# Optimization experiments

Hardware: AMD Instinct MI355X
Metric: run time of the kernel (lower is better)

## Reference

```python
import jax, jax.numpy as jnp
import numpy as np

EPS = 1e-12


def agnn_layer(x, row, col, num_nodes):
    """AGNN propagation with beta frozen at 1.0 (requires_grad=False in source).
    alpha_ij = softmax_{j in N(i)} ( beta * cos(x_i, x_j) ); out_i = sum_j alpha_ij * x_j.
    row = destination node of each edge (segment id), col = source node.
    """
    xn = x / (jnp.linalg.norm(x, axis=-1, keepdims=True) + EPS)  # unit-norm features
    score = jnp.sum(xn[row] * xn[col], axis=-1)                   # [E] beta=1 * cos sim
    smax = jax.ops.segment_max(score, row, num_segments=num_nodes)
    e = jnp.exp(score - smax[row])                                # stable softmax numerator
    denom = jax.ops.segment_sum(e, row, num_segments=num_nodes)
    alpha = e / jnp.maximum(denom[row], EPS)                      # [E]
    out = jax.ops.segment_sum(alpha[:, None] * x[col], row, num_segments=num_nodes)
    return out


def setup_inputs() -> dict:
    key = jax.random.key(0)
    ks = jax.random.split(key, 8)
    N, E = 100000, 1600000
    IN_DIM, HID, OUT_DIM = 128, 64, 64
    x = jax.random.normal(ks[0], (N, IN_DIM), dtype=jnp.float32)
    edge_row = jnp.sort(jax.random.randint(ks[1], (E,), 0, N))
    edge_col = jax.random.randint(ks[2], (E,), 0, N)
    # Linear params (PyTorch nn.Linear style: y = x @ W.T + b)
    s1 = 1.0 / np.sqrt(IN_DIM)
    W1 = jax.random.uniform(ks[3], (HID, IN_DIM), jnp.float32, -s1, s1)
    b1 = jax.random.uniform(ks[4], (HID,), jnp.float32, -s1, s1)
    s2 = 1.0 / np.sqrt(HID)
    W2 = jax.random.uniform(ks[5], (OUT_DIM, HID), jnp.float32, -s2, s2)
    b2 = jax.random.uniform(ks[6], (OUT_DIM,), jnp.float32, -s2, s2)
    return {"x": x, "edge_row": edge_row, "edge_col": edge_col,
            "W1": W1, "b1": b1, "W2": W2, "b2": b2}


def reference(x, edge_row, edge_col, W1, b1, W2, b2):
    N = x.shape[0]
    h = jax.nn.relu(x @ W1.T + b1)
    for _ in range(4):  # 4 frozen-beta AGNN layers
        h = jax.nn.relu(agnn_layer(h, edge_row, edge_col, N))
    return h @ W2.T + b2
```

## Files before the change

kernel.cpp:

```cpp
#include <hip/hip_runtime.h>


typedef float v2f __attribute__((ext_vector_type(2)));

#define DEV_INLINE __device__ __forceinline__

DEV_INLINE v2f bf2(unsigned u) {
    v2f r;
    r.x = __uint_as_float(u << 16);
    r.y = __uint_as_float(u & 0xffff0000u);
    return r;
}

DEV_INLINE unsigned pack_bf16_2(float a, float b) {
    unsigned ua = __float_as_uint(a); ua += 0x7fffu + ((ua >> 16) & 1u);
    unsigned ub = __float_as_uint(b); ub += 0x7fffu + ((ub >> 16) & 1u);
    return (ua >> 16) | (ub & 0xffff0000u);
}

template <int CTRL>
DEV_INLINE float dpp_add(float v) {
    int sh = __builtin_amdgcn_update_dpp(0, __float_as_int(v), CTRL, 0xF, 0xF, true);
    return v + __int_as_float(sh);
}
DEV_INLINE float group8_sum_bcast(float v) {
    float r = dpp_add<0x111>(v);
    r = dpp_add<0x112>(r);
    r = dpp_add<0x114>(r);
    return __int_as_float(__builtin_amdgcn_ds_swizzle(__float_as_int(r), 0x00F8));
}

__global__ __launch_bounds__(256) void build_rowptr(const int* __restrict__ row,
                                                    int* __restrict__ ptr,
                                                    int N, int E) {
    int i = blockIdx.x * blockDim.x + threadIdx.x;
    if (i > N) return;
    int lo = 0, hi = E;
    while (lo < hi) {
        int mid = (lo + hi) >> 1;
        if (row[mid] < i) lo = mid + 1; else hi = mid;
    }
    ptr[i] = lo;
}

__global__ __launch_bounds__(256) void gemm1_relu(const float* __restrict__ x,
                                                  const float* __restrict__ W1,
                                                  const float* __restrict__ b1,
                                                  unsigned short* __restrict__ xn,
                                                  float* __restrict__ nrm,
                                                  int N) {
    __shared__ __align__(16) float Wt[64 * 64];
    __shared__ __align__(16) float xT[64 * 64];
    const int tid  = threadIdx.x;
    const int tx   = tid & 15;
    const int ty   = tid >> 4;
    const int base = blockIdx.x * 64;

    float4 b4 = ((const float4*)b1)[tx];
    float4 acc[4];
    acc[0] = b4; acc[1] = b4; acc[2] = b4; acc[3] = b4;

    for (int kc = 0; kc < 128; kc += 64) {
        if (kc) __syncthreads();
        const float4* W4 = (const float4*)W1;
        for (int idx = tid; idx < 64 * 16; idx += 256) {
            int o = idx & 63, k4 = idx >> 6;
            float4 v = W4[o * 32 + (kc >> 2) + k4];
            Wt[(4 * k4 + 0) * 64 + o] = v.x;
            Wt[(4 * k4 + 1) * 64 + o] = v.y;
            Wt[(4 * k4 + 2) * 64 + o] = v.z;
            Wt[(4 * k4 + 3) * 64 + o] = v.w;
        }
        const float4* x4p = (const float4*)x;
        for (int idx = tid; idx < 64 * 16; idx += 256) {
            int mm = idx & 63, k4 = idx >> 6;
            int node = base + mm;
            float4 v = make_float4(0.f, 0.f, 0.f, 0.f);
            if (node < N) v = x4p[(size_t)node * 32 + (kc >> 2) + k4];
            xT[(4 * k4 + 0) * 64 + mm] = v.x;
            xT[(4 * k4 + 1) * 64 + mm] = v.y;
            xT[(4 * k4 + 2) * 64 + mm] = v.z;
            xT[(4 * k4 + 3) * 64 + mm] = v.w;
        }
        __syncthreads();

#pragma unroll 4
        for (int k = 0; k < 64; ++k) {
            const float4 w4 = *(const float4*)&Wt[k * 64 + 4 * tx];
            const float4 xv = *(const float4*)&xT[k * 64 + 4 * ty];
            acc[0].x = fmaf(xv.x, w4.x, acc[0].x);
            acc[0].y = fmaf(xv.x, w4.y, acc[0].y);
            acc[0].z = fmaf(xv.x, w4.z, acc[0].z);
            acc[0].w = fmaf(xv.x, w4.w, acc[0].w);
            acc[1].x = fmaf(xv.y, w4.x, acc[1].x);
            acc[1].y = fmaf(xv.y, w4.y, acc[1].y);
            acc[1].z = fmaf(xv.y, w4.z, acc[1].z);
            acc[1].w = fmaf(xv.y, w4.w, acc[1].w);
            acc[2].x = fmaf(xv.z, w4.x, acc[2].x);
            acc[2].y = fmaf(xv.z, w4.y, acc[2].y);
            acc[2].z = fmaf(xv.z, w4.z, acc[2].z);
            acc[2].w = fmaf(xv.z, w4.w, acc[2].w);
            acc[3].x = fmaf(xv.w, w4.x, acc[3].x);
            acc[3].y = fmaf(xv.w, w4.y, acc[3].y);
            acc[3].z = fmaf(xv.w, w4.z, acc[3].z);
            acc[3].w = fmaf(xv.w, w4.w, acc[3].w);
        }
    }

#pragma unroll
    for (int mm = 0; mm < 4; ++mm) {
        float4 r = acc[mm];
        r.x = fmaxf(r.x, 0.f); r.y = fmaxf(r.y, 0.f);
        r.z = fmaxf(r.z, 0.f); r.w = fmaxf(r.w, 0.f);
        float s = fmaf(r.x, r.x, fmaf(r.y, r.y, fmaf(r.z, r.z, r.w * r.w)));
        s += __shfl_xor(s, 1, 64);
        s += __shfl_xor(s, 2, 64);
        s += __shfl_xor(s, 4, 64);
        s += __shfl_xor(s, 8, 64);
        const float nn  = sqrtf(s) + 1e-12f;
        const float inv = 1.f / nn;
        int node = base + 4 * ty + mm;
        if (node < N) {
            uint2 pk;
            pk.x = pack_bf16_2(r.x * inv, r.y * inv);
            pk.y = pack_bf16_2(r.z * inv, r.w * inv);
            *(uint2*)&xn[(size_t)node * 64 + 4 * tx] = pk;
            if (tx == mm) nrm[node] = nn;
        }
    }
}

__global__ __launch_bounds__(256) void agnn_layer(const uint4* __restrict__ xn4,
                                                  const float* __restrict__ nrm,
                                                  const int* __restrict__ ptr,
                                                  const int* __restrict__ col,
                                                  uint4* __restrict__ xo4,
                                                  float* __restrict__ nrmo,
                                                  int N) {
    const int tid  = threadIdx.x;
    const int lane = tid & 63;
    const int g    = (lane >> 3) & 3;
    const int sub  = lane & 7;
    const int i    = blockIdx.x * 8 + (tid >> 5);
    if (i >= N) return;

    const float L2E = 1.4426950408889634f;
    const uint4 hv = xn4[(size_t)i * 8 + sub];
    v2f hi0 = bf2(hv.x), hi1 = bf2(hv.y), hi2v = bf2(hv.z), hi3 = bf2(hv.w);
    hi0 *= L2E; hi1 *= L2E; hi2v *= L2E; hi3 *= L2E;

    const int p0 = ptr[i], p1 = ptr[i + 1];

    float den = 0.f;
    v2f a0 = {0.f, 0.f}, a1 = {0.f, 0.f}, a2 = {0.f, 0.f}, a3 = {0.f, 0.f};

#define EDGE_BODY(V, NRMJ)                                                   \
    {                                                                        \
        v2f x0 = bf2((V).x), x1 = bf2((V).y), x2 = bf2((V).z), x3 = bf2((V).w); \
        v2f s2v = hi0 * x0; s2v += hi1 * x1; s2v += hi2v * x2; s2v += hi3 * x3; \
        const float p = exp2f(group8_sum_bcast(s2v.x + s2v.y));              \
        den += p;                                                            \
        const float wp = p * (NRMJ);                                         \
        v2f w2 = {wp, wp};                                                   \
        a0 += w2 * x0; a1 += w2 * x1; a2 += w2 * x2; a3 += w2 * x3;          \
    }

    int e = p0 + g;
    for (; e + 12 < p1; e += 16) {
        const int j0 = col[e];
        const int j1 = col[e + 4];
        const int j2 = col[e + 8];
        const int j3 = col[e + 12];
        const uint4 v0 = xn4[(size_t)j0 * 8 + sub];
        const uint4 v1 = xn4[(size_t)j1 * 8 + sub];
        const uint4 v2 = xn4[(size_t)j2 * 8 + sub];
        const uint4 v3 = xn4[(size_t)j3 * 8 + sub];
        const float n0 = nrm[j0];
        const float n1 = nrm[j1];
        const float n2 = nrm[j2];
        const float n3 = nrm[j3];
        EDGE_BODY(v0, n0)
        EDGE_BODY(v1, n1)
        EDGE_BODY(v2, n2)
        EDGE_BODY(v3, n3)
    }
    for (; e < p1; e += 4) {
        const int j = col[e];
        const uint4 v = xn4[(size_t)j * 8 + sub];
        const float nj = nrm[j];
        EDGE_BODY(v, nj)
    }
#undef EDGE_BODY

#pragma unroll
    for (int off = 8; off <= 16; off <<= 1) {
        den  += __shfl_xor(den, off, 64);
        a0.x += __shfl_xor(a0.x, off, 64);  a0.y += __shfl_xor(a0.y, off, 64);
        a1.x += __shfl_xor(a1.x, off, 64);  a1.y += __shfl_xor(a1.y, off, 64);
        a2.x += __shfl_xor(a2.x, off, 64);  a2.y += __shfl_xor(a2.y, off, 64);
        a3.x += __shfl_xor(a3.x, off, 64);  a3.y += __shfl_xor(a3.y, off, 64);
    }

    const float id = 1.f / fmaxf(den, 1e-12f);
    float o[8];
    o[0] = fmaxf(a0.x * id, 0.f); o[1] = fmaxf(a0.y * id, 0.f);
    o[2] = fmaxf(a1.x * id, 0.f); o[3] = fmaxf(a1.y * id, 0.f);
    o[4] = fmaxf(a2.x * id, 0.f); o[5] = fmaxf(a2.y * id, 0.f);
    o[6] = fmaxf(a3.x * id, 0.f); o[7] = fmaxf(a3.y * id, 0.f);

    float s2 = 0.f;
#pragma unroll
    for (int t = 0; t < 8; ++t) s2 = fmaf(o[t], o[t], s2);
    s2 += __shfl_xor(s2, 1, 64);
    s2 += __shfl_xor(s2, 2, 64);
    s2 += __shfl_xor(s2, 4, 64);
    const float nn  = sqrtf(s2) + 1e-12f;
    const float inv = 1.f / nn;

    if (g == 0) {
        uint4 ov;
        ov.x = pack_bf16_2(o[0] * inv, o[1] * inv);
        ov.y = pack_bf16_2(o[2] * inv, o[3] * inv);
        ov.z = pack_bf16_2(o[4] * inv, o[5] * inv);
        ov.w = pack_bf16_2(o[6] * inv, o[7] * inv);
        xo4[(size_t)i * 8 + sub] = ov;
        if (sub == 0) nrmo[i] = nn;
    }
}

__global__ __launch_bounds__(256) void gemm2(const unsigned short* __restrict__ xn,
                                             const float* __restrict__ nrm,
                                             const float* __restrict__ W2,
                                             const float* __restrict__ b2,
                                             float* __restrict__ out,
                                             int N) {
    __shared__ __align__(16) float Wt[64 * 64];
    __shared__ __align__(16) float xT[64 * 64];
    const int tid  = threadIdx.x;
    const int tx   = tid & 15;
    const int ty   = tid >> 4;
    const int base = blockIdx.x * 64;

    {
        const float4* W4 = (const float4*)W2;
        for (int idx = tid; idx < 64 * 16; idx += 256) {
            int o = idx & 63, k4 = idx >> 6;
            float4 v = W4[o * 16 + k4];
            Wt[(4 * k4 + 0) * 64 + o] = v.x;
            Wt[(4 * k4 + 1) * 64 + o] = v.y;
            Wt[(4 * k4 + 2) * 64 + o] = v.z;
            Wt[(4 * k4 + 3) * 64 + o] = v.w;
        }
        const uint2* x2 = (const uint2*)xn;
        for (int idx = tid; idx < 64 * 16; idx += 256) {
            int mm = idx & 63, k4 = idx >> 6;
            int node = base + mm;
            uint2 v = make_uint2(0u, 0u);
            float nn = 0.f;
            if (node < N) { v = x2[(size_t)node * 16 + k4]; nn = nrm[node]; }
            xT[(4 * k4 + 0) * 64 + mm] = __uint_as_float(v.x << 16) * nn;
            xT[(4 * k4 + 1) * 64 + mm] = __uint_as_float(v.x & 0xffff0000u) * nn;
            xT[(4 * k4 + 2) * 64 + mm] = __uint_as_float(v.y << 16) * nn;
            xT[(4 * k4 + 3) * 64 + mm] = __uint_as_float(v.y & 0xffff0000u) * nn;
        }
    }
    __syncthreads();

    float4 b4 = ((const float4*)b2)[tx];
    float4 acc[4];
    acc[0] = b4; acc[1] = b4; acc[2] = b4; acc[3] = b4;

#pragma unroll 4
    for (int k = 0; k < 64; ++k) {
        const float4 w4 = *(const float4*)&Wt[k * 64 + 4 * tx];
        const float4 xv = *(const float4*)&xT[k * 64 + 4 * ty];
        acc[0].x = fmaf(xv.x, w4.x, acc[0].x);
        acc[0].y = fmaf(xv.x, w4.y, acc[0].y);
        acc[0].z = fmaf(xv.x, w4.z, acc[0].z);
        acc[0].w = fmaf(xv.x, w4.w, acc[0].w);
        acc[1].x = fmaf(xv.y, w4.x, acc[1].x);
        acc[1].y = fmaf(xv.y, w4.y, acc[1].y);
        acc[1].z = fmaf(xv.y, w4.z, acc[1].z);
        acc[1].w = fmaf(xv.y, w4.w, acc[1].w);
        acc[2].x = fmaf(xv.z, w4.x, acc[2].x);
        acc[2].y = fmaf(xv.z, w4.y, acc[2].y);
        acc[2].z = fmaf(xv.z, w4.z, acc[2].z);
        acc[2].w = fmaf(xv.z, w4.w, acc[2].w);
        acc[3].x = fmaf(xv.w, w4.x, acc[3].x);
        acc[3].y = fmaf(xv.w, w4.y, acc[3].y);
        acc[3].z = fmaf(xv.w, w4.z, acc[3].z);
        acc[3].w = fmaf(xv.w, w4.w, acc[3].w);
    }

#pragma unroll
    for (int mm = 0; mm < 4; ++mm) {
        int node = base + 4 * ty + mm;
        if (node < N) *(float4*)&out[(size_t)node * 64 + 4 * tx] = acc[mm];
    }
}

extern "C" void kernel_launch(void* const* d_in, const int* in_sizes, int n_in,
                              void* d_out, int out_size, void* d_ws, size_t ws_size,
                              hipStream_t stream) {
    const float* x   = (const float*)d_in[0];
    const int*   row = (const int*)d_in[1];
    const int*   col = (const int*)d_in[2];
    const float* W1  = (const float*)d_in[3];
    const float* b1  = (const float*)d_in[4];
    const float* W2  = (const float*)d_in[5];
    const float* b2  = (const float*)d_in[6];
    float* out = (float*)d_out;

    const int N = in_sizes[0] / 128;
    const int E = in_sizes[1];

    char* ws = (char*)d_ws;
    size_t off = 0;
    unsigned short* ha = (unsigned short*)(ws + off); off += (size_t)N * 64 * 2;
    unsigned short* hb = (unsigned short*)(ws + off); off += (size_t)N * 64 * 2;
    float* na_ = (float*)(ws + off); off += (size_t)N * sizeof(float);
    float* nb_ = (float*)(ws + off); off += (size_t)N * sizeof(float);
    int*   ptr = (int*)  (ws + off); off += (size_t)(N + 1) * sizeof(int);
    (void)ws_size; (void)n_in; (void)out_size;

    build_rowptr<<<(N + 256) / 256, 256, 0, stream>>>(row, ptr, N, E);

    const int nbG = (N + 63) / 64;
    gemm1_relu<<<nbG, 256, 0, stream>>>(x, W1, b1, ha, na_, N);

    const int nb8 = (N + 7) / 8;
    unsigned short* hc = ha; unsigned short* hn = hb;
    float* nc = na_; float* nn = nb_;
    for (int l = 0; l < 4; ++l) {
        agnn_layer<<<nb8, 256, 0, stream>>>((const uint4*)hc, nc, ptr, col,
                                            (uint4*)hn, nn, N);
        unsigned short* t = hc; hc = hn; hn = t;
        float* tf = nc; nc = nn; nn = tf;
    }

    gemm2<<<nbG, 256, 0, stream>>>(hc, nc, W2, b2, out, N);
}
```

Measured before the change: 336.6 us.

## Switch stored features from bf16 to fp16 and use packed fp16 dot/accumulate

New measurement: 306.1 us. -9.0%, faster.

```diff
diff --git a/kernel.cpp b/kernel.cpp
--- a/kernel.cpp
+++ b/kernel.cpp
@@ -1,33 +1,16 @@
 #include <hip/hip_runtime.h>
 
 
-typedef float v2f __attribute__((ext_vector_type(2)));
+typedef _Float16 h2 __attribute__((ext_vector_type(2)));
+
+union U4H { uint4 u; h2 h[4]; };
+union U2H { uint2 u; h2 h[2]; };
+union UHI { unsigned u; h2 h; };
 
 #define DEV_INLINE __device__ __forceinline__
 
-DEV_INLINE v2f bf2(unsigned u) {
-    v2f r;
-    r.x = __uint_as_float(u << 16);
-    r.y = __uint_as_float(u & 0xffff0000u);
-    return r;
-}
-
-DEV_INLINE unsigned pack_bf16_2(float a, float b) {
-    unsigned ua = __float_as_uint(a); ua += 0x7fffu + ((ua >> 16) & 1u);
-    unsigned ub = __float_as_uint(b); ub += 0x7fffu + ((ub >> 16) & 1u);
-    return (ua >> 16) | (ub & 0xffff0000u);
-}
-
-template <int CTRL>
-DEV_INLINE float dpp_add(float v) {
-    int sh = __builtin_amdgcn_update_dpp(0, __float_as_int(v), CTRL, 0xF, 0xF, true);
-    return v + __int_as_float(sh);
-}
-DEV_INLINE float group8_sum_bcast(float v) {
-    float r = dpp_add<0x111>(v);
-    r = dpp_add<0x112>(r);
-    r = dpp_add<0x114>(r);
-    return __int_as_float(__builtin_amdgcn_ds_swizzle(__float_as_int(r), 0x00F8));
+DEV_INLINE h2 mkh2(float a, float b) {
+    h2 r; r.x = (_Float16)a; r.y = (_Float16)b; return r;
 }
 
 __global__ __launch_bounds__(256) void build_rowptr(const int* __restrict__ row,
@@ -121,10 +104,10 @@
         const float inv = 1.f / nn;
         int node = base + 4 * ty + mm;
         if (node < N) {
-            uint2 pk;
-            pk.x = pack_bf16_2(r.x * inv, r.y * inv);
-            pk.y = pack_bf16_2(r.z * inv, r.w * inv);
-            *(uint2*)&xn[(size_t)node * 64 + 4 * tx] = pk;
+            U2H pk;
+            pk.h[0] = mkh2(r.x * inv, r.y * inv);
+            pk.h[1] = mkh2(r.z * inv, r.w * inv);
+            *(uint2*)&xn[(size_t)node * 64 + 4 * tx] = pk.u;
             if (tx == mm) nrm[node] = nn;
         }
     }
@@ -144,49 +127,57 @@
     const int i    = blockIdx.x * 8 + (tid >> 5);
     if (i >= N) return;
 
-    const float L2E = 1.4426950408889634f;
-    const uint4 hv = xn4[(size_t)i * 8 + sub];
-    v2f hi0 = bf2(hv.x), hi1 = bf2(hv.y), hi2v = bf2(hv.z), hi3 = bf2(hv.w);
-    hi0 *= L2E; hi1 *= L2E; hi2v *= L2E; hi3 *= L2E;
+    U4H hi_;
+    hi_.u = xn4[(unsigned)i * 8u + sub];
+    {
+        const _Float16 L2E = (_Float16)1.4426950408889634f;
+        h2 l2 = {L2E, L2E};
+#pragma unroll
+        for (int t = 0; t < 4; ++t) hi_.h[t] *= l2;
+    }
 
     const int p0 = ptr[i], p1 = ptr[i + 1];
 
     float den = 0.f;
-    v2f a0 = {0.f, 0.f}, a1 = {0.f, 0.f}, a2 = {0.f, 0.f}, a3 = {0.f, 0.f};
-
-#define EDGE_BODY(V, NRMJ)                                                   \
+    U4H acc;
+    acc.h[0] = mkh2(0.f, 0.f); acc.h[1] = mkh2(0.f, 0.f);
+    acc.h[2] = mkh2(0.f, 0.f); acc.h[3] = mkh2(0.f, 0.f);
+
+#define EDGE_BODY(VU, NRMJ)                                                  \
     {                                                                        \
-        v2f x0 = bf2((V).x), x1 = bf2((V).y), x2 = bf2((V).z), x3 = bf2((V).w); \
-        v2f s2v = hi0 * x0; s2v += hi1 * x1; s2v += hi2v * x2; s2v += hi3 * x3; \
-        const float p = exp2f(group8_sum_bcast(s2v.x + s2v.y));              \
+        U4H xa; xa.u = (VU);                                                 \
+        float s = 0.f;                                                       \
+        s = __builtin_amdgcn_fdot2(hi_.h[0], xa.h[0], s, false);             \
+        s = __builtin_amdgcn_fdot2(hi_.h[1], xa.h[1], s, false);             \
+        s = __builtin_amdgcn_fdot2(hi_.h[2], xa.h[2], s, false);             \
+        s = __builtin_amdgcn_fdot2(hi_.h[3], xa.h[3], s, false);             \
+        s += __shfl_xor(s, 1, 64);                                           \
+        s += __shfl_xor(s, 2, 64);                                           \
+        s += __shfl_xor(s, 4, 64);                                           \
+        const float p = exp2f(s);                                            \
         den += p;                                                            \
-        const float wp = p * (NRMJ);                                         \
-        v2f w2 = {wp, wp};                                                   \
-        a0 += w2 * x0; a1 += w2 * x1; a2 += w2 * x2; a3 += w2 * x3;          \
+        const _Float16 wh = (_Float16)(p * (NRMJ));                          \
+        h2 w2 = {wh, wh};                                                    \
+        acc.h[0] += w2 * xa.h[0];                                            \
+        acc.h[1] += w2 * xa.h[1];                                            \
+        acc.h[2] += w2 * xa.h[2];                                            \
+        acc.h[3] += w2 * xa.h[3];                                            \
     }
 
     int e = p0 + g;
-    for (; e + 12 < p1; e += 16) {
-        const int j0 = col[e];
-        const int j1 = col[e + 4];
-        const int j2 = col[e + 8];
-        const int j3 = col[e + 12];
-        const uint4 v0 = xn4[(size_t)j0 * 8 + sub];
-        const uint4 v1 = xn4[(size_t)j1 * 8 + sub];
-        const uint4 v2 = xn4[(size_t)j2 * 8 + sub];
-        const uint4 v3 = xn4[(size_t)j3 * 8 + sub];
-        const float n0 = nrm[j0];
-        const float n1 = nrm[j1];
-        const float n2 = nrm[j2];
-        const float n3 = nrm[j3];
-        EDGE_BODY(v0, n0)
-        EDGE_BODY(v1, n1)
-        EDGE_BODY(v2, n2)
-        EDGE_BODY(v3, n3)
-    }
-    for (; e < p1; e += 4) {
+    for (; e + 4 < p1; e += 8) {
+        const int ja = col[e];
+        const int jb = col[e + 4];
+        const uint4 va = xn4[(unsigned)ja * 8u + sub];
+        const uint4 vb = xn4[(unsigned)jb * 8u + sub];
+        const float na = nrm[ja];
+        const float nb = nrm[jb];
+        EDGE_BODY(va, na)
+        EDGE_BODY(vb, nb)
+    }
+    if (e < p1) {
         const int j = col[e];
-        const uint4 v = xn4[(size_t)j * 8 + sub];
+        const uint4 v = xn4[(unsigned)j * 8u + sub];
         const float nj = nrm[j];
         EDGE_BODY(v, nj)
     }
@@ -194,19 +185,22 @@
 
 #pragma unroll
     for (int off = 8; off <= 16; off <<= 1) {
-        den  += __shfl_xor(den, off, 64);
-        a0.x += __shfl_xor(a0.x, off, 64);  a0.y += __shfl_xor(a0.y, off, 64);
-        a1.x += __shfl_xor(a1.x, off, 64);  a1.y += __shfl_xor(a1.y, off, 64);
-        a2.x += __shfl_xor(a2.x, off, 64);  a2.y += __shfl_xor(a2.y, off, 64);
-        a3.x += __shfl_xor(a3.x, off, 64);  a3.y += __shfl_xor(a3.y, off, 64);
+        den += __shfl_xor(den, off, 64);
+#pragma unroll
+        for (int t = 0; t < 4; ++t) {
+            UHI a; a.h = acc.h[t];
+            UHI b; b.u = (unsigned)__shfl_xor((int)a.u, off, 64);
+            acc.h[t] = a.h + b.h;
+        }
     }
 
     const float id = 1.f / fmaxf(den, 1e-12f);
     float o[8];
-    o[0] = fmaxf(a0.x * id, 0.f); o[1] = fmaxf(a0.y * id, 0.f);
-    o[2] = fmaxf(a1.x * id, 0.f); o[3] = fmaxf(a1.y * id, 0.f);
-    o[4] = fmaxf(a2.x * id, 0.f); o[5] = fmaxf(a2.y * id, 0.f);
-    o[6] = fmaxf(a3.x * id, 0.f); o[7] = fmaxf(a3.y * id, 0.f);
+#pragma unroll
+    for (int t = 0; t < 4; ++t) {
+        o[2 * t]     = fmaxf((float)acc.h[t].x * id, 0.f);
+        o[2 * t + 1] = fmaxf((float)acc.h[t].y * id, 0.f);
+    }
 
     float s2 = 0.f;
 #pragma unroll
@@ -218,12 +212,12 @@
     const float inv = 1.f / nn;
 
     if (g == 0) {
-        uint4 ov;
-        ov.x = pack_bf16_2(o[0] * inv, o[1] * inv);
-        ov.y = pack_bf16_2(o[2] * inv, o[3] * inv);
-        ov.z = pack_bf16_2(o[4] * inv, o[5] * inv);
-        ov.w = pack_bf16_2(o[6] * inv, o[7] * inv);
-        xo4[(size_t)i * 8 + sub] = ov;
+        U4H ov;
+        ov.h[0] = mkh2(o[0] * inv, o[1] * inv);
+        ov.h[1] = mkh2(o[2] * inv, o[3] * inv);
+        ov.h[2] = mkh2(o[4] * inv, o[5] * inv);
+        ov.h[3] = mkh2(o[6] * inv, o[7] * inv);
+        xo4[(unsigned)i * 8u + sub] = ov.u;
         if (sub == 0) nrmo[i] = nn;
     }
 }
@@ -255,13 +249,13 @@
         for (int idx = tid; idx < 64 * 16; idx += 256) {
             int mm = idx & 63, k4 = idx >> 6;
             int node = base + mm;
-            uint2 v = make_uint2(0u, 0u);
+            U2H v; v.u = make_uint2(0u, 0u);
             float nn = 0.f;
-            if (node < N) { v = x2[(size_t)node * 16 + k4]; nn = nrm[node]; }
-            xT[(4 * k4 + 0) * 64 + mm] = __uint_as_float(v.x << 16) * nn;
-            xT[(4 * k4 + 1) * 64 + mm] = __uint_as_float(v.x & 0xffff0000u) * nn;
-            xT[(4 * k4 + 2) * 64 + mm] = __uint_as_float(v.y << 16) * nn;
-            xT[(4 * k4 + 3) * 64 + mm] = __uint_as_float(v.y & 0xffff0000u) * nn;
+            if (node < N) { v.u = x2[(size_t)node * 16 + k4]; nn = nrm[node]; }
+            xT[(4 * k4 + 0) * 64 + mm] = (float)v.h[0].x * nn;
+            xT[(4 * k4 + 1) * 64 + mm] = (float)v.h[0].y * nn;
+            xT[(4 * k4 + 2) * 64 + mm] = (float)v.h[1].x * nn;
+            xT[(4 * k4 + 3) * 64 + mm] = (float)v.h[1].y * nn;
         }
     }
     __syncthreads();
```
